# Performance work log

Hardware: AMD Instinct MI355X
Metric: run time of the kernel (lower is better)

The kernel has to match this reference:

```python
import jax, jax.numpy as jnp
import numpy as np
import math

B = 512          # graphs per batch
NP = 200         # nodes per graph
E_PER = 2000     # edges per graph
V = 50000        # item vocab
EMB = 9
HID = 128
RATIO = 0.8
K1 = math.ceil(RATIO * NP)   # 160
K2 = math.ceil(RATIO * K1)   # 128
K3 = math.ceil(RATIO * K2)   # 103


def sage_conv(x, src, dst, valid, n, w_neigh, w_root, b):
    # PyG SAGEConv: lin_l(mean_{j->i} x_j) + lin_r(x_i) + bias
    msg = x[src] * valid[:, None]                      # [E, C]
    seg = jnp.where(valid > 0, dst, n)                 # invalid edges -> dummy segment
    s = jax.ops.segment_sum(msg, seg, num_segments=n + 1)[:n]
    cnt = jax.ops.segment_sum(valid, seg, num_segments=n + 1)[:n]
    mean = s / jnp.maximum(cnt, 1.0)[:, None]
    return mean @ w_neigh.T + x @ w_root.T + b


def topk_pool(x, src, dst, valid, np_cur, k, p):
    # TopKPooling: score = tanh(x.p/||p||); keep top-k per graph; x *= score
    n = x.shape[0]
    score = jnp.tanh((x @ p) / jnp.linalg.norm(p))
    topv, topi = jax.lax.top_k(score.reshape(B, np_cur), k)   # [B, k]
    kept = (jnp.arange(B)[:, None] * np_cur + topi).reshape(-1)
    n_new = B * k
    x_new = x[kept] * topv.reshape(-1)[:, None]
    mapping = jnp.full((n,), -1, dtype=jnp.int32).at[kept].set(
        jnp.arange(n_new, dtype=jnp.int32))
    ns, nd = mapping[src], mapping[dst]
    valid_new = valid * ((ns >= 0) & (nd >= 0)).astype(valid.dtype)
    return x_new, jnp.maximum(ns, 0), jnp.maximum(nd, 0), valid_new


def global_pool(x, k):
    # cat([global_max_pool, global_mean_pool]) with uniform graph size k
    xr = x.reshape(B, k, -1)
    return jnp.concatenate([xr.max(axis=1), xr.mean(axis=1)], axis=1)


def setup_inputs() -> dict:
    key = jax.random.key(0)
    ks = jax.random.split(key, 24)
    # block-structured intra-graph edges
    s = jax.random.randint(ks[0], (B, E_PER), 0, NP)
    d = jax.random.randint(ks[1], (B, E_PER), 0, NP)
    off = (jnp.arange(B) * NP)[:, None]
    edge_index = jnp.stack([(s + off).reshape(-1), (d + off).reshape(-1)]).astype(jnp.int32)
    node_ids = jax.random.randint(ks[2], (B * NP, 1), 0, V)
    batch = jnp.repeat(jnp.arange(B), NP)
    sc = 0.1
    p = {
        'emb': jax.random.normal(ks[3], (V, EMB)) * sc,
        'w1n': jax.random.normal(ks[4], (HID, EMB)) * sc,
        'w1r': jax.random.normal(ks[5], (HID, EMB)) * sc,
        'b1': jnp.zeros((HID,)),
        'w2n': jax.random.normal(ks[6], (HID, HID)) * sc,
        'w2r': jax.random.normal(ks[7], (HID, HID)) * sc,
        'b2': jnp.zeros((HID,)),
        'w3n': jax.random.normal(ks[8], (HID, HID)) * sc,
        'w3r': jax.random.normal(ks[9], (HID, HID)) * sc,
        'b3': jnp.zeros((HID,)),
        'p1': jax.random.normal(ks[10], (HID,)) * sc,
        'p2': jax.random.normal(ks[11], (HID,)) * sc,
        'p3': jax.random.normal(ks[12], (HID,)) * sc,
        'lw1': jax.random.normal(ks[13], (HID, 2 * HID)) * sc,
        'lb1': jnp.zeros((HID,)),
        'lw2': jax.random.normal(ks[14], (64, HID)) * sc,
        'lb2': jnp.zeros((64,)),
        'lw3': jax.random.normal(ks[15], (1, 64)) * sc,
        'lb3': jnp.zeros((1,)),
    }
    return {'node_ids': node_ids, 'edge_index': edge_index, 'batch': batch, **p}


def reference(node_ids, edge_index, batch, emb, w1n, w1r, b1, w2n, w2r, b2,
              w3n, w3r, b3, p1, p2, p3, lw1, lb1, lw2, lb2, lw3, lb3):
    src, dst = edge_index[0], edge_index[1]
    valid = jnp.ones(src.shape[0], dtype=jnp.float32)
    x = emb[node_ids[:, 0]]                                  # [N, 9]
    x = jax.nn.relu(sage_conv(x, src, dst, valid, B * NP, w1n, w1r, b1))
    x, src, dst, valid = topk_pool(x, src, dst, valid, NP, K1, p1)
    x1 = global_pool(x, K1)
    x = jax.nn.relu(sage_conv(x, src, dst, valid, B * K1, w2n, w2r, b2))
    x, src, dst, valid = topk_pool(x, src, dst, valid, K1, K2, p2)
    x2 = global_pool(x, K2)
    x = jax.nn.relu(sage_conv(x, src, dst, valid, B * K2, w3n, w3r, b3))
    x, src, dst, valid = topk_pool(x, src, dst, valid, K2, K3, p3)
    x3 = global_pool(x, K3)
    h = x1 + x2 + x3                                         # [B, 256]
    h = jax.nn.relu(h @ lw1.T + lb1)
    h = jax.nn.relu(h @ lw2.T + lb2)
    return jax.nn.sigmoid(h @ lw3.T + lb3)[:, 0]             # [B]
```

## Files before the change

### kernel.cpp

```cpp
#include <hip/hip_runtime.h>
#include <math.h>

constexpr int B    = 512;
constexpr int NPG  = 200;
constexpr int EPER = 2000;
constexpr int EMB  = 9;
constexpr int HID  = 128;
constexpr int K1   = 160;
constexpr int K2   = 128;
constexpr int K3   = 103;
constexpr int E    = B * EPER;

__device__ __forceinline__ void scan_off(const int* deg, int* off2,
                                         int lane, int wv) {
    if (wv == 0) {
        int i0 = lane * 4;
        int v0 = deg[i0], v1 = deg[i0 + 1], v2 = deg[i0 + 2], v3 = deg[i0 + 3];
        int s1 = v0 + v1, s2 = s1 + v2, s3 = s2 + v3;
        int run = s3;
        #pragma unroll
        for (int o = 1; o < 64; o <<= 1) {
            int t = __shfl_up(run, o, 64);
            if (lane >= o) run += t;
        }
        int excl = run - s3;
        off2[i0]     = excl;
        off2[i0 + 1] = excl + v0;
        off2[i0 + 2] = excl + s1;
        off2[i0 + 3] = excl + s2;
        if (lane == 63) off2[256] = run;
    }
}

__global__ __launch_bounds__(640, 2) void k_fused(
        const int* __restrict__ node_ids,
        const float* __restrict__ emb,
        const int* __restrict__ es, const int* __restrict__ ed,
        const float* __restrict__ w1n, const float* __restrict__ w1r,
        const float* __restrict__ b1, const float* __restrict__ p1,
        const float* __restrict__ w2n, const float* __restrict__ w2r,
        const float* __restrict__ b2, const float* __restrict__ p2,
        const float* __restrict__ w3n, const float* __restrict__ w3r,
        const float* __restrict__ b3, const float* __restrict__ p3,
        float* __restrict__ g1, float* __restrict__ g2,
        float* __restrict__ g3) {
    const int g = blockIdx.x, tid = threadIdx.x;
    const int lane = tid & 63, wv = tid >> 6;

    __shared__ float xY[K1 * 132];
    __shared__ float S[2 * 32 * 132];
    __shared__ int   csr[EPER];
    __shared__ int   deg[256], off2[257], cur[256];
    __shared__ int   idsL[NPG];
    __shared__ float sc[NPG];
    __shared__ int   pos1[NPG], pos2[K1], inv2[K2];

    const int eb = g * EPER, nb0 = g * NPG;

    {
        float* x0L  = S;
        float* mnL  = S + 1800;
        float* redA = S + 3600;
        if (tid < NPG) idsL[tid] = node_ids[g * NPG + tid];
        if (tid < 256) deg[tid] = 0;
        __syncthreads();
        for (int i = tid; i < NPG * EMB; i += 640) {
            int n = i / EMB, j = i - n * EMB;
            x0L[i] = emb[(size_t)idsL[n] * EMB + j];
        }
        for (int e = tid; e < EPER; e += 640)
            atomicAdd(&deg[ed[eb + e] - nb0], 1);
        __syncthreads();
        scan_off(deg, off2, lane, wv);
        __syncthreads();
        if (tid < 256) cur[tid] = off2[tid];
        __syncthreads();
        for (int e = tid; e < EPER; e += 640) {
            int slot = atomicAdd(&cur[ed[eb + e] - nb0], 1);
            csr[slot] = es[eb + e] - nb0;
        }
        __syncthreads();
        if (tid < NPG) {
            int bg = off2[tid], en = off2[tid + 1];
            float a[EMB];
            #pragma unroll
            for (int j = 0; j < EMB; j++) a[j] = 0.f;
            for (int t = bg; t < en; t++) {
                int s = csr[t];
                #pragma unroll
                for (int j = 0; j < EMB; j++) a[j] += x0L[s * EMB + j];
            }
            float inv = 1.f / (float)((en - bg) > 1 ? (en - bg) : 1);
            #pragma unroll
            for (int j = 0; j < EMB; j++) mnL[tid * EMB + j] = a[j] * inv;
        }
        float pl0 = p1[lane], pl1 = p1[64 + lane];
        float pp = pl0 * pl0 + pl1 * pl1;
        #pragma unroll
        for (int o = 32; o >= 1; o >>= 1) pp += __shfl_xor(pp, o, 64);
        float nrm = sqrtf(pp);
        float wn0[EMB], wn1[EMB], wr0[EMB], wr1[EMB];
        #pragma unroll
        for (int j = 0; j < EMB; j++) {
            wn0[j] = w1n[lane * EMB + j];
            wn1[j] = w1n[(lane + 64) * EMB + j];
            wr0[j] = w1r[lane * EMB + j];
            wr1[j] = w1r[(lane + 64) * EMB + j];
        }
        float bb0 = b1[lane], bb1 = b1[64 + lane];
        __syncthreads();
        for (int i = wv; i < NPG; i += 10) {
            float c0 = bb0, c1 = bb1;
            #pragma unroll
            for (int j = 0; j < EMB; j++) {
                float m = mnL[i * EMB + j];
                float x = x0L[i * EMB + j];
                c0 += m * wn0[j] + x * wr0[j];
                c1 += m * wn1[j] + x * wr1[j];
            }
            c0 = fmaxf(c0, 0.f);
            c1 = fmaxf(c1, 0.f);
            float d = c0 * pl0 + c1 * pl1;
            #pragma unroll
            for (int o = 32; o >= 1; o >>= 1) d += __shfl_xor(d, o, 64);
            if (lane == 0) sc[i] = tanhf(d / nrm);
        }
        __syncthreads();
        if (tid < NPG) {
            float scv = sc[tid];
            int rank = 0;
            for (int j = 0; j < NPG; j++) {
                float o = sc[j];
                rank += (o > scv) || (o == scv && j < tid);
            }
            pos1[tid] = (rank < K1) ? rank : -1;
        }
        __syncthreads();
        float pm0 = -INFINITY, pm1 = -INFINITY, ps0 = 0.f, ps1 = 0.f;
        for (int i = wv; i < NPG; i += 10) {
            int r = pos1[i];
            if (r < 0) continue;
            float c0 = bb0, c1 = bb1;
            #pragma unroll
            for (int j = 0; j < EMB; j++) {
                float m = mnL[i * EMB + j];
                float x = x0L[i * EMB + j];
                c0 += m * wn0[j] + x * wr0[j];
                c1 += m * wn1[j] + x * wr1[j];
            }
            float s = sc[i];
            float v0 = fmaxf(c0, 0.f) * s;
            float v1 = fmaxf(c1, 0.f) * s;
            xY[r * 132 + lane] = v0;
            xY[r * 132 + 64 + lane] = v1;
            pm0 = fmaxf(pm0, v0); ps0 += v0;
            pm1 = fmaxf(pm1, v1); ps1 += v1;
        }
        redA[wv * 128 + lane] = pm0;
        redA[wv * 128 + 64 + lane] = pm1;
        redA[1280 + wv * 128 + lane] = ps0;
        redA[1280 + wv * 128 + 64 + lane] = ps1;
        __syncthreads();
        if (tid < 128) {
            float mx = redA[tid], sm = redA[1280 + tid];
            #pragma unroll
            for (int w = 1; w < 10; w++) {
                mx = fmaxf(mx, redA[w * 128 + tid]);
                sm += redA[1280 + w * 128 + tid];
            }
            g1[g * 256 + tid] = mx;
            g1[g * 256 + 128 + tid] = sm / (float)K1;
        }
        __syncthreads();
    }

    {
        if (tid < 256) deg[tid] = 0;
        __syncthreads();
        for (int e = tid; e < EPER; e += 640) {
            int a = pos1[es[eb + e] - nb0];
            int b = pos1[ed[eb + e] - nb0];
            if (a >= 0 && b >= 0) atomicAdd(&deg[b], 1);
        }
        __syncthreads();
        scan_off(deg, off2, lane, wv);
        __syncthreads();
        if (tid < 256) cur[tid] = off2[tid];
        __syncthreads();
        for (int e = tid; e < EPER; e += 640) {
            int a = pos1[es[eb + e] - nb0];
            int b = pos1[ed[eb + e] - nb0];
            if (a >= 0 && b >= 0) {
                int slot = atomicAdd(&cur[b], 1);
                csr[slot] = a;
            }
        }
        __syncthreads();

        const int tc = tid & 31, tr = tid >> 5;
        float accY[8][4], accZ[8][4];
        #pragma unroll
        for (int r = 0; r < 8; r++)
            #pragma unroll
            for (int c = 0; c < 4; c++) { accY[r][c] = 0.f; accZ[r][c] = 0.f; }

        const int sr = tid >> 3, sc4 = (tid & 7) * 4;
        const bool stager = (sr < 64);
        const float* wsrc0 = (sr < 32) ? w2n : w2r;
        const int wrow = (sr < 32) ? sr : sr - 32;
        float* Bmine = S + ((sr < 32) ? 0 : 32 * 132);
        float4 bvv[4];
        if (stager) {
            #pragma unroll
            for (int i = 0; i < 4; i++)
                bvv[i] = *(const float4*)(wsrc0 + (size_t)(wrow + i * 32) * HID + sc4);
        }
        for (int ch = 0; ch < 4; ch++) {
            if (stager) {
                #pragma unroll
                for (int i = 0; i < 4; i++) {
                    int r = wrow + i * 32;
                    Bmine[(sc4 + 0) * 132 + r] = bvv[i].x;
                    Bmine[(sc4 + 1) * 132 + r] = bvv[i].y;
                    Bmine[(sc4 + 2) * 132 + r] = bvv[i].z;
                    Bmine[(sc4 + 3) * 132 + r] = bvv[i].w;
                }
            }
            __syncthreads();
            if (ch + 1 < 4 && stager) {
                #pragma unroll
                for (int i = 0; i < 4; i++)
                    bvv[i] = *(const float4*)(wsrc0 + (size_t)(wrow + i * 32) * HID
                                              + (ch + 1) * 32 + sc4);
            }
            for (int kq = 0; kq < 8; kq++) {
                float4 af[8];
                #pragma unroll
                for (int rr = 0; rr < 8; rr++)
                    af[rr] = *(const float4*)&xY[(tr * 8 + rr) * 132 + ch * 32 + kq * 4];
                #pragma unroll
                for (int kk = 0; kk < 4; kk++) {
                    int k = kq * 4 + kk;
                    float4 bn = *(const float4*)&S[k * 132 + tc * 4];
                    float4 br = *(const float4*)&S[32 * 132 + k * 132 + tc * 4];
                    #pragma unroll
                    for (int rr = 0; rr < 8; rr++) {
                        float a = (kk == 0) ? af[rr].x : (kk == 1) ? af[rr].y
                                 : (kk == 2) ? af[rr].z : af[rr].w;
                        accY[rr][0] += a * bn.x; accY[rr][1] += a * bn.y;
                        accY[rr][2] += a * bn.z; accY[rr][3] += a * bn.w;
                        accZ[rr][0] += a * br.x; accZ[rr][1] += a * br.y;
                        accZ[rr][2] += a * br.z; accZ[rr][3] += a * br.w;
                    }
                }
            }
            __syncthreads();
        }
        #pragma unroll
        for (int rr = 0; rr < 8; rr++) {
            float4 yv = {accY[rr][0], accY[rr][1], accY[rr][2], accY[rr][3]};
            *(float4*)&xY[(tr * 8 + rr) * 132 + tc * 4] = yv;
        }
        __syncthreads();

        float bias[4], pv[4];
        #pragma unroll
        for (int c = 0; c < 4; c++) {
            bias[c] = b2[tc * 4 + c];
            pv[c]   = p2[tc * 4 + c];
        }
        float a0 = p2[lane], a1 = p2[64 + lane];
        float pp = a0 * a0 + a1 * a1;
        #pragma unroll
        for (int o = 32; o >= 1; o >>= 1) pp += __shfl_xor(pp, o, 64);
        float nrm = sqrtf(pp);
        float outv[8][4];
        #pragma unroll
        for (int rr = 0; rr < 8; rr++) {
            int m = tr * 8 + rr;
            int bg = off2[m], en = off2[m + 1];
            float s0 = 0.f, s1 = 0.f, s2 = 0.f, s3 = 0.f;
            for (int t = bg; t < en; t++) {
                float4 yv = *(const float4*)&xY[csr[t] * 132 + tc * 4];
                s0 += yv.x; s1 += yv.y; s2 += yv.z; s3 += yv.w;
            }
            float inv = 1.f / (float)((en - bg) > 1 ? (en - bg) : 1);
            outv[rr][0] = fmaxf(s0 * inv + accZ[rr][0] + bias[0], 0.f);
            outv[rr][1] = fmaxf(s1 * inv + accZ[rr][1] + bias[1], 0.f);
            outv[rr][2] = fmaxf(s2 * inv + accZ[rr][2] + bias[2], 0.f);
            outv[rr][3] = fmaxf(s3 * inv + accZ[rr][3] + bias[3], 0.f);
        }
        float* scpart = S;
        #pragma unroll
        for (int rr = 0; rr < 8; rr++) {
            float sp = outv[rr][0] * pv[0] + outv[rr][1] * pv[1]
                     + outv[rr][2] * pv[2] + outv[rr][3] * pv[3];
            scpart[(tr * 8 + rr) * 32 + tc] = sp;
        }
        __syncthreads();
        #pragma unroll
        for (int rr = 0; rr < 8; rr++) {
            float4 ov = {outv[rr][0], outv[rr][1], outv[rr][2], outv[rr][3]};
            *(float4*)&xY[(tr * 8 + rr) * 132 + tc * 4] = ov;
        }
        __syncthreads();
        if (tid < K1) {
            float sum = 0.f;
            #pragma unroll
            for (int t = 0; t < 32; t++) sum += scpart[tid * 32 + t];
            sc[tid] = tanhf(sum / nrm);
        }
        __syncthreads();
        if (tid < K1) {
            float scv = sc[tid];
            int rank = 0;
            for (int j = 0; j < K1; j++) {
                float o = sc[j];
                rank += (o > scv) || (o == scv && j < tid);
            }
            pos2[tid] = (rank < K2) ? rank : -1;
            if (rank < K2) inv2[rank] = tid;
        }
        __syncthreads();
        float cm[4], cs[4];
        #pragma unroll
        for (int c = 0; c < 4; c++) { cm[c] = -INFINITY; cs[c] = 0.f; }
        #pragma unroll
        for (int rr = 0; rr < 8; rr++) {
            int m = tr * 8 + rr;
            int r = pos2[m];
            if (r < 0) continue;
            float sv = sc[m];
            float4 ov = *(const float4*)&xY[m * 132 + tc * 4];
            ov.x *= sv; ov.y *= sv; ov.z *= sv; ov.w *= sv;
            *(float4*)&xY[m * 132 + tc * 4] = ov;
            cm[0] = fmaxf(cm[0], ov.x); cs[0] += ov.x;
            cm[1] = fmaxf(cm[1], ov.y); cs[1] += ov.y;
            cm[2] = fmaxf(cm[2], ov.z); cs[2] += ov.z;
            cm[3] = fmaxf(cm[3], ov.w); cs[3] += ov.w;
        }
        __syncthreads();
        float* redM = S;
        float* redS = S + 20 * 128;
        #pragma unroll
        for (int c = 0; c < 4; c++) {
            redM[tr * 128 + tc * 4 + c] = cm[c];
            redS[tr * 128 + tc * 4 + c] = cs[c];
        }
        __syncthreads();
        if (tid < 128) {
            float mx = redM[tid], sm = redS[tid];
            #pragma unroll 4
            for (int t = 1; t < 20; t++) {
                mx = fmaxf(mx, redM[t * 128 + tid]);
                sm += redS[t * 128 + tid];
            }
            g2[g * 256 + tid] = mx;
            g2[g * 256 + 128 + tid] = sm / (float)K2;
        }
        __syncthreads();
    }

    {
        if (tid < 256) deg[tid] = 0;
        __syncthreads();
        for (int e = tid; e < EPER; e += 640) {
            int a = pos1[es[eb + e] - nb0];
            int b = pos1[ed[eb + e] - nb0];
            a = (a >= 0) ? pos2[a] : -1;
            b = (b >= 0) ? pos2[b] : -1;
            if (a >= 0 && b >= 0) atomicAdd(&deg[b], 1);
        }
        __syncthreads();
        scan_off(deg, off2, lane, wv);
        __syncthreads();
        if (tid < 256) cur[tid] = off2[tid];
        __syncthreads();
        for (int e = tid; e < EPER; e += 640) {
            int a = pos1[es[eb + e] - nb0];
            int b = pos1[ed[eb + e] - nb0];
            a = (a >= 0) ? pos2[a] : -1;
            b = (b >= 0) ? pos2[b] : -1;
            if (a >= 0 && b >= 0) {
                int slot = atomicAdd(&cur[b], 1);
                csr[slot] = a;
            }
        }
        __syncthreads();

        const int tc = tid & 31, tr = tid >> 5;
        const bool comp = (tid < 512);
        int srcrow[8];
        if (comp) {
            #pragma unroll
            for (int rr = 0; rr < 8; rr++) srcrow[rr] = inv2[tr * 8 + rr];
        }
        float accY[8][4], accZ[8][4];
        #pragma unroll
        for (int r = 0; r < 8; r++)
            #pragma unroll
            for (int c = 0; c < 4; c++) { accY[r][c] = 0.f; accZ[r][c] = 0.f; }

        const int sr = tid >> 3, sc4 = (tid & 7) * 4;
        const bool stager = (sr < 64);
        const float* wsrc0 = (sr < 32) ? w3n : w3r;
        const int wrow = (sr < 32) ? sr : sr - 32;
        float* Bmine = S + ((sr < 32) ? 0 : 32 * 132);
        float4 bvv[4];
        if (stager) {
            #pragma unroll
            for (int i = 0; i < 4; i++)
                bvv[i] = *(const float4*)(wsrc0 + (size_t)(wrow + i * 32) * HID + sc4);
        }
        for (int ch = 0; ch < 4; ch++) {
            if (stager) {
                #pragma unroll
                for (int i = 0; i < 4; i++) {
                    int r = wrow + i * 32;
                    Bmine[(sc4 + 0) * 132 + r] = bvv[i].x;
                    Bmine[(sc4 + 1) * 132 + r] = bvv[i].y;
                    Bmine[(sc4 + 2) * 132 + r] = bvv[i].z;
                    Bmine[(sc4 + 3) * 132 + r] = bvv[i].w;
                }
            }
            __syncthreads();
            if (ch + 1 < 4 && stager) {
                #pragma unroll
                for (int i = 0; i < 4; i++)
                    bvv[i] = *(const float4*)(wsrc0 + (size_t)(wrow + i * 32) * HID
                                              + (ch + 1) * 32 + sc4);
            }
            if (comp) {
                for (int kq = 0; kq < 8; kq++) {
                    float4 af[8];
                    #pragma unroll
                    for (int rr = 0; rr < 8; rr++)
                        af[rr] = *(const float4*)&xY[srcrow[rr] * 132 + ch * 32 + kq * 4];
                    #pragma unroll
                    for (int kk = 0; kk < 4; kk++) {
                        int k = kq * 4 + kk;
                        float4 bn = *(const float4*)&S[k * 132 + tc * 4];
                        float4 br = *(const float4*)&S[32 * 132 + k * 132 + tc * 4];
                        #pragma unroll
                        for (int rr = 0; rr < 8; rr++) {
                            float a = (kk == 0) ? af[rr].x : (kk == 1) ? af[rr].y
                                     : (kk == 2) ? af[rr].z : af[rr].w;
                            accY[rr][0] += a * bn.x; accY[rr][1] += a * bn.y;
                            accY[rr][2] += a * bn.z; accY[rr][3] += a * bn.w;
                            accZ[rr][0] += a * br.x; accZ[rr][1] += a * br.y;
                            accZ[rr][2] += a * br.z; accZ[rr][3] += a * br.w;
                        }
                    }
                }
            }
            __syncthreads();
        }
        if (comp) {
            #pragma unroll
            for (int rr = 0; rr < 8; rr++) {
                float4 yv = {accY[rr][0], accY[rr][1], accY[rr][2], accY[rr][3]};
                *(float4*)&xY[(tr * 8 + rr) * 132 + tc * 4] = yv;
            }
        }
        __syncthreads();

        float bias[4], pv[4];
        #pragma unroll
        for (int c = 0; c < 4; c++) {
            bias[c] = b3[tc * 4 + c];
            pv[c]   = p3[tc * 4 + c];
        }
        float a0 = p3[lane], a1 = p3[64 + lane];
        float pp = a0 * a0 + a1 * a1;
        #pragma unroll
        for (int o = 32; o >= 1; o >>= 1) pp += __shfl_xor(pp, o, 64);
        float nrm = sqrtf(pp);
        float outv[8][4];
        float* scpart = S;
        if (comp) {
            #pragma unroll
            for (int rr = 0; rr < 8; rr++) {
                int m = tr * 8 + rr;
                int bg = off2[m], en = off2[m + 1];
                float s0 = 0.f, s1 = 0.f, s2 = 0.f, s3 = 0.f;
                for (int t = bg; t < en; t++) {
                    float4 yv = *(const float4*)&xY[csr[t] * 132 + tc * 4];
                    s0 += yv.x; s1 += yv.y; s2 += yv.z; s3 += yv.w;
                }
                float inv = 1.f / (float)((en - bg) > 1 ? (en - bg) : 1);
                outv[rr][0] = fmaxf(s0 * inv + accZ[rr][0] + bias[0], 0.f);
                outv[rr][1] = fmaxf(s1 * inv + accZ[rr][1] + bias[1], 0.f);
                outv[rr][2] = fmaxf(s2 * inv + accZ[rr][2] + bias[2], 0.f);
                outv[rr][3] = fmaxf(s3 * inv + accZ[rr][3] + bias[3], 0.f);
            }
            #pragma unroll
            for (int rr = 0; rr < 8; rr++) {
                float sp = outv[rr][0] * pv[0] + outv[rr][1] * pv[1]
                         + outv[rr][2] * pv[2] + outv[rr][3] * pv[3];
                scpart[(tr * 8 + rr) * 32 + tc] = sp;
            }
        }
        __syncthreads();
        if (comp) {
            #pragma unroll
            for (int rr = 0; rr < 8; rr++) {
                float4 ov = {outv[rr][0], outv[rr][1], outv[rr][2], outv[rr][3]};
                *(float4*)&xY[(tr * 8 + rr) * 132 + tc * 4] = ov;
            }
        }
        __syncthreads();
        if (tid < K2) {
            float sum = 0.f;
            #pragma unroll
            for (int t = 0; t < 32; t++) sum += scpart[tid * 32 + t];
            sc[tid] = tanhf(sum / nrm);
        }
        __syncthreads();
        int* posC = idsL;
        if (tid < K2) {
            float scv = sc[tid];
            int rank = 0;
            for (int j = 0; j < K2; j++) {
                float o = sc[j];
                rank += (o > scv) || (o == scv && j < tid);
            }
            posC[tid] = (rank < K3) ? rank : -1;
        }
        __syncthreads();
        float cm[4], cs[4];
        #pragma unroll
        for (int c = 0; c < 4; c++) { cm[c] = -INFINITY; cs[c] = 0.f; }
        if (comp) {
            #pragma unroll
            for (int rr = 0; rr < 8; rr++) {
                int m = tr * 8 + rr;
                int r = posC[m];
                if (r < 0) continue;
                float sv = sc[m];
                float4 ov = *(const float4*)&xY[m * 132 + tc * 4];
                cm[0] = fmaxf(cm[0], ov.x * sv); cs[0] += ov.x * sv;
                cm[1] = fmaxf(cm[1], ov.y * sv); cs[1] += ov.y * sv;
                cm[2] = fmaxf(cm[2], ov.z * sv); cs[2] += ov.z * sv;
                cm[3] = fmaxf(cm[3], ov.w * sv); cs[3] += ov.w * sv;
            }
        }
        __syncthreads();
        float* redM = S;
        float* redS = S + 16 * 128;
        if (comp) {
            #pragma unroll
            for (int c = 0; c < 4; c++) {
                redM[tr * 128 + tc * 4 + c] = cm[c];
                redS[tr * 128 + tc * 4 + c] = cs[c];
            }
        }
        __syncthreads();
        if (tid < 128) {
            float mx = redM[tid], sm = redS[tid];
            #pragma unroll 4
            for (int t = 1; t < 16; t++) {
                mx = fmaxf(mx, redM[t * 128 + tid]);
                sm += redS[t * 128 + tid];
            }
            g3[g * 256 + tid] = mx;
            g3[g * 256 + 128 + tid] = sm / (float)K3;
        }
    }
}

__global__ __launch_bounds__(128) void k_mlp(const float* __restrict__ g1, const float* __restrict__ g2,
                      const float* __restrict__ g3,
                      const float* __restrict__ lw1, const float* __restrict__ lb1,
                      const float* __restrict__ lw2, const float* __restrict__ lb2,
                      const float* __restrict__ lw3, const float* __restrict__ lb3,
                      float* __restrict__ out) {
    int g = blockIdx.x, t = threadIdx.x;
    __shared__ float h0[256];
    __shared__ float h1[128];
    __shared__ float h2r[64];
    h0[t]       = g1[g * 256 + t] + g2[g * 256 + t] + g3[g * 256 + t];
    h0[t + 128] = g1[g * 256 + 128 + t] + g2[g * 256 + 128 + t] + g3[g * 256 + 128 + t];
    __syncthreads();
    float a = lb1[t];
    #pragma unroll 4
    for (int j = 0; j < 256; j++) a += h0[j] * lw1[t * 256 + j];
    h1[t] = fmaxf(a, 0.f);
    __syncthreads();
    if (t < 64) {
        float a2 = lb2[t];
        #pragma unroll 4
        for (int j = 0; j < 128; j++) a2 += h1[j] * lw2[t * 128 + j];
        h2r[t] = fmaxf(a2, 0.f) * lw3[t];
    }
    __syncthreads();
    if (t == 0) {
        float s = 0.f;
        for (int j = 0; j < 64; j++) s += h2r[j];
        s += lb3[0];
        out[g] = 1.f / (1.f + expf(-s));
    }
}

extern "C" void kernel_launch(void* const* d_in, const int* in_sizes, int n_in,
                              void* d_out, int out_size, void* d_ws, size_t ws_size,
                              hipStream_t stream) {
    const int*   node_ids = (const int*)d_in[0];
    const int*   ei   = (const int*)d_in[1];
    const float* emb  = (const float*)d_in[3];
    const float* w1n  = (const float*)d_in[4];
    const float* w1r  = (const float*)d_in[5];
    const float* b1   = (const float*)d_in[6];
    const float* w2n  = (const float*)d_in[7];
    const float* w2r  = (const float*)d_in[8];
    const float* b2   = (const float*)d_in[9];
    const float* w3n  = (const float*)d_in[10];
    const float* w3r  = (const float*)d_in[11];
    const float* b3   = (const float*)d_in[12];
    const float* p1   = (const float*)d_in[13];
    const float* p2   = (const float*)d_in[14];
    const float* p3   = (const float*)d_in[15];
    const float* lw1  = (const float*)d_in[16];
    const float* lb1  = (const float*)d_in[17];
    const float* lw2  = (const float*)d_in[18];
    const float* lb2  = (const float*)d_in[19];
    const float* lw3  = (const float*)d_in[20];
    const float* lb3  = (const float*)d_in[21];
    float* out = (float*)d_out;

    float* ws  = (float*)d_ws;
    float* g1  = ws;
    float* g2  = g1 + B * 2 * HID;
    float* g3  = g2 + B * 2 * HID;

    k_fused<<<B, 640, 0, stream>>>(node_ids, emb, ei, ei + E,
                                   w1n, w1r, b1, p1,
                                   w2n, w2r, b2, p2,
                                   w3n, w3r, b3, p3,
                                   g1, g2, g3);
    k_mlp<<<B, 128, 0, stream>>>(g1, g2, g3, lw1, lb1, lw2, lb2, lw3, lb3, out);
}
```

Baseline: 369.2 us.

## Compact pooled rows in shared memory and pool from registers instead of reloading

Stage 2's scaled outputs are now written directly to their compacted rank slot in shared memory. This removes the inv2 indirection table and the indexed row gather in the stage-3 GEMM. The global max/mean pooling now reads from the outv registers rather than reloading xY, and the unscaled write-back plus two barriers are dropped. The launch bounds are loosened from 2 to 1 blocks per SM, giving the compiler more registers at the cost of possibly lower occupancy.

```diff
diff --git a/kernel.cpp b/kernel.cpp
--- a/kernel.cpp
+++ b/kernel.cpp
@@ -32,7 +32,7 @@
     }
 }
 
-__global__ __launch_bounds__(640, 2) void k_fused(
+__global__ __launch_bounds__(640, 1) void k_fused(
         const int* __restrict__ node_ids,
         const float* __restrict__ emb,
         const int* __restrict__ es, const int* __restrict__ ed,
@@ -53,7 +53,7 @@
     __shared__ int   deg[256], off2[257], cur[256];
     __shared__ int   idsL[NPG];
     __shared__ float sc[NPG];
-    __shared__ int   pos1[NPG], pos2[K1], inv2[K2];
+    __shared__ int   pos1[NPG], pos2[K1];
 
     const int eb = g * EPER, nb0 = g * NPG;
 
@@ -291,17 +291,12 @@
             outv[rr][3] = fmaxf(s3 * inv + accZ[rr][3] + bias[3], 0.f);
         }
         float* scpart = S;
+        __syncthreads();
         #pragma unroll
         for (int rr = 0; rr < 8; rr++) {
             float sp = outv[rr][0] * pv[0] + outv[rr][1] * pv[1]
                      + outv[rr][2] * pv[2] + outv[rr][3] * pv[3];
             scpart[(tr * 8 + rr) * 32 + tc] = sp;
-        }
-        __syncthreads();
-        #pragma unroll
-        for (int rr = 0; rr < 8; rr++) {
-            float4 ov = {outv[rr][0], outv[rr][1], outv[rr][2], outv[rr][3]};
-            *(float4*)&xY[(tr * 8 + rr) * 132 + tc * 4] = ov;
         }
         __syncthreads();
         if (tid < K1) {
@@ -319,7 +314,6 @@
                 rank += (o > scv) || (o == scv && j < tid);
             }
             pos2[tid] = (rank < K2) ? rank : -1;
-            if (rank < K2) inv2[rank] = tid;
         }
         __syncthreads();
         float cm[4], cs[4];
@@ -331,15 +325,15 @@
             int r = pos2[m];
             if (r < 0) continue;
             float sv = sc[m];
-            float4 ov = *(const float4*)&xY[m * 132 + tc * 4];
-            ov.x *= sv; ov.y *= sv; ov.z *= sv; ov.w *= sv;
-            *(float4*)&xY[m * 132 + tc * 4] = ov;
-            cm[0] = fmaxf(cm[0], ov.x); cs[0] += ov.x;
-            cm[1] = fmaxf(cm[1], ov.y); cs[1] += ov.y;
-            cm[2] = fmaxf(cm[2], ov.z); cs[2] += ov.z;
-            cm[3] = fmaxf(cm[3], ov.w); cs[3] += ov.w;
-        }
-        __syncthreads();
+            float v0 = outv[rr][0] * sv, v1 = outv[rr][1] * sv;
+            float v2 = outv[rr][2] * sv, v3 = outv[rr][3] * sv;
+            cm[0] = fmaxf(cm[0], v0); cs[0] += v0;
+            cm[1] = fmaxf(cm[1], v1); cs[1] += v1;
+            cm[2] = fmaxf(cm[2], v2); cs[2] += v2;
+            cm[3] = fmaxf(cm[3], v3); cs[3] += v3;
+            float4 o0 = {v0, v1, v2, v3};
+            *(float4*)&xY[r * 132 + tc * 4] = o0;
+        }
         float* redM = S;
         float* redS = S + 20 * 128;
         #pragma unroll
@@ -390,11 +384,6 @@
 
         const int tc = tid & 31, tr = tid >> 5;
         const bool comp = (tid < 512);
-        int srcrow[8];
-        if (comp) {
-            #pragma unroll
-            for (int rr = 0; rr < 8; rr++) srcrow[rr] = inv2[tr * 8 + rr];
-        }
         float accY[8][4], accZ[8][4];
         #pragma unroll
         for (int r = 0; r < 8; r++)
@@ -435,7 +424,7 @@
                     float4 af[8];
                     #pragma unroll
                     for (int rr = 0; rr < 8; rr++)
-                        af[rr] = *(const float4*)&xY[srcrow[rr] * 132 + ch * 32 + kq * 4];
+                        af[rr] = *(const float4*)&xY[(tr * 8 + rr) * 132 + ch * 32 + kq * 4];
                     #pragma unroll
                     for (int kk = 0; kk < 4; kk++) {
                         int k = kq * 4 + kk;
@@ -493,19 +482,14 @@
                 outv[rr][2] = fmaxf(s2 * inv + accZ[rr][2] + bias[2], 0.f);
                 outv[rr][3] = fmaxf(s3 * inv + accZ[rr][3] + bias[3], 0.f);
             }
+        }
+        __syncthreads();
+        if (comp) {
             #pragma unroll
             for (int rr = 0; rr < 8; rr++) {
                 float sp = outv[rr][0] * pv[0] + outv[rr][1] * pv[1]
                          + outv[rr][2] * pv[2] + outv[rr][3] * pv[3];
                 scpart[(tr * 8 + rr) * 32 + tc] = sp;
-            }
-        }
-        __syncthreads();
-        if (comp) {
-            #pragma unroll
-            for (int rr = 0; rr < 8; rr++) {
-                float4 ov = {outv[rr][0], outv[rr][1], outv[rr][2], outv[rr][3]};
-                *(float4*)&xY[(tr * 8 + rr) * 132 + tc * 4] = ov;
             }
         }
         __syncthreads();
@@ -537,14 +521,14 @@
                 int r = posC[m];
                 if (r < 0) continue;
                 float sv = sc[m];
-                float4 ov = *(const float4*)&xY[m * 132 + tc * 4];
-                cm[0] = fmaxf(cm[0], ov.x * sv); cs[0] += ov.x * sv;
-                cm[1] = fmaxf(cm[1], ov.y * sv); cs[1] += ov.y * sv;
-                cm[2] = fmaxf(cm[2], ov.z * sv); cs[2] += ov.z * sv;
-                cm[3] = fmaxf(cm[3], ov.w * sv); cs[3] += ov.w * sv;
-            }
-        }
-        __syncthreads();
+                #pragma unroll
+                for (int c = 0; c < 4; c++) {
+                    float v = outv[rr][c] * sv;
+                    cm[c] = fmaxf(cm[c], v);
+                    cs[c] += v;
+                }
+            }
+        }
         float* redM = S;
         float* redS = S + 16 * 128;
         if (comp) {
```

Measured after the change: 359.0 us. 2.8% less time.
